# Kernel optimization log

Measured on AMD Instinct MI355X. Metric: run time of the kernel, lower is better.

The kernel has to match this reference:

```python
import jax, jax.numpy as jnp
import numpy as np

D = 384      # n_embed_dims
H = 6        # n_heads
HS = D // H  # head_size = 64
T = 256      # block_size
B = 256
EPS = 1e-5


def setup_inputs() -> dict:
    key = jax.random.key(0)
    ks = jax.random.split(key, 12)
    s_in = 1.0 / np.sqrt(D)
    s_ff = 1.0 / np.sqrt(4 * D)
    return {
        "x": jax.random.normal(ks[0], (B, T, D), jnp.float32),
        # per-head QKV weights, stacked [H, D, HS] (Linear bias=False)
        "wq": jax.random.normal(ks[1], (H, D, HS), jnp.float32) * s_in,
        "wk": jax.random.normal(ks[2], (H, D, HS), jnp.float32) * s_in,
        "wv": jax.random.normal(ks[3], (H, D, HS), jnp.float32) * s_in,
        "w_proj": jax.random.normal(ks[4], (D, D), jnp.float32) * s_in,
        "b_proj": jax.random.normal(ks[5], (D,), jnp.float32) * s_in,
        "w1": jax.random.normal(ks[6], (D, 4 * D), jnp.float32) * s_in,
        "b1": jax.random.normal(ks[7], (4 * D,), jnp.float32) * s_in,
        "w2": jax.random.normal(ks[8], (4 * D, D), jnp.float32) * s_ff,
        "b2": jax.random.normal(ks[9], (D,), jnp.float32) * s_ff,
        "g1": jnp.ones((D,), jnp.float32),
        "be1": jnp.zeros((D,), jnp.float32),
        "g2": jnp.ones((D,), jnp.float32),
        "be2": jnp.zeros((D,), jnp.float32),
    }


def _layernorm(x, g, b):
    mu = jnp.mean(x, axis=-1, keepdims=True)
    var = jnp.mean(jnp.square(x - mu), axis=-1, keepdims=True)
    return (x - mu) * jax.lax.rsqrt(var + EPS) * g + b


def _attention(x, wq, wk, wv, w_proj, b_proj):
    # faithful quirk: scale = 1/sqrt(C) with C = full embed dim (384)
    scale = 1.0 / jnp.sqrt(jnp.asarray(D, x.dtype))
    q = jnp.einsum("btd,hde->bhte", x, wq)  # [B,H,T,HS]
    k = jnp.einsum("btd,hde->bhte", x, wk)
    v = jnp.einsum("btd,hde->bhte", x, wv)
    w = jnp.einsum("bhte,bhse->bhts", q, k) * scale  # [B,H,T,T], no mask
    w = jax.nn.softmax(w, axis=-1)
    out = jnp.einsum("bhts,bhse->bhte", w, v)  # [B,H,T,HS]
    # concat heads along feature dim (head order matches torch cat)
    out = out.transpose(0, 2, 1, 3).reshape(x.shape[0], x.shape[1], D)
    return out @ w_proj + b_proj


def reference(x, wq, wk, wv, w_proj, b_proj, w1, b1, w2, b2, g1, be1, g2, be2):
    x = x + _attention(_layernorm(x, g1, be1), wq, wk, wv, w_proj, b_proj)
    h = _layernorm(x, g2, be2)
    h = jax.nn.relu(h @ w1 + b1) @ w2 + b2  # dropout = eval-mode identity
    return x + h
```

## Files before the change

### kernel.cpp

```cpp
#include <hip/hip_runtime.h>
#include <stdint.h>

#define NTOK 65536
#define DE 384
#define QSTR 1280

typedef __bf16 bf16x8 __attribute__((ext_vector_type(8)));
typedef float  f32x4  __attribute__((ext_vector_type(4)));
typedef float  f32x16 __attribute__((ext_vector_type(16)));
typedef unsigned short u16x8 __attribute__((ext_vector_type(8)));

__device__ __forceinline__ unsigned short f2bf(float f) {
  union { float fl; unsigned u; } a; a.fl = f;
  unsigned r = a.u + 0x7fffu + ((a.u >> 16) & 1u);
  return (unsigned short)(r >> 16);
}
__device__ __forceinline__ float b2f(unsigned short s) {
  union { unsigned u; float f; } v; v.u = (unsigned)s << 16; return v.f;
}

__device__ __forceinline__ void gll16(const void* g, void* l) {
  __builtin_amdgcn_global_load_lds((const __attribute__((address_space(1))) void*)g,
                                   (__attribute__((address_space(3))) void*)l, 16, 0, 0);
}

__device__ __forceinline__ bf16x8 ds128(unsigned addr) {
  bf16x8 r;
  asm volatile("ds_read_b128 %0, %1" : "=v"(r) : "v"(addr));
  return r;
}

__global__ void pack_t(unsigned short* __restrict__ dst, const float* __restrict__ src,
                       int R, int C) {
  int t = blockIdx.x * 256 + threadIdx.x;
  if (t >= R * C) return;
  int r = t / C, c = t - r * C;
  dst[(size_t)c * R + r] = f2bf(src[t]);
}

__global__ void qkv_pack(const float* __restrict__ wq, const float* __restrict__ wk,
                         const float* __restrict__ wv, unsigned short* __restrict__ dst) {
  int t = blockIdx.x * 256 + threadIdx.x;
  if (t >= QSTR * 384) return;
  int n = t / 384, k = t - n * 384;
  unsigned short v = 0;
  if (n < 1152) {
    int which = n / 384, r = n - which * 384;
    const float* src = which == 0 ? wq : (which == 1 ? wk : wv);
    int h = r >> 6, e = r & 63;
    v = f2bf(src[h * 24576 + k * 64 + e]);
  }
  dst[t] = v;
}

__global__ __launch_bounds__(256) void ln_kernel(const float* __restrict__ x,
                                                 const float* __restrict__ g,
                                                 const float* __restrict__ be,
                                                 unsigned short* __restrict__ out) {
  int wave = threadIdx.x >> 6, lane = threadIdx.x & 63;
  size_t row = (size_t)blockIdx.x * 4 + wave;
  const float* xr = x + row * DE;
  int c0 = lane * 2;
  float2 v0 = *(const float2*)(xr + c0);
  float2 v1 = *(const float2*)(xr + 128 + c0);
  float2 v2 = *(const float2*)(xr + 256 + c0);
  float s  = v0.x + v0.y + v1.x + v1.y + v2.x + v2.y;
  float ss = v0.x*v0.x + v0.y*v0.y + v1.x*v1.x + v1.y*v1.y + v2.x*v2.x + v2.y*v2.y;
#pragma unroll
  for (int m = 1; m < 64; m <<= 1) { s += __shfl_xor(s, m); ss += __shfl_xor(ss, m); }
  float mu = s * (1.0f / 384.0f);
  float rstd = rsqrtf(ss * (1.0f / 384.0f) - mu * mu + 1e-5f);
  unsigned short* orow = out + row * DE;
  {
    float a0 = (v0.x - mu) * rstd * g[c0] + be[c0];
    float a1 = (v0.y - mu) * rstd * g[c0 + 1] + be[c0 + 1];
    *(unsigned*)(orow + c0) = (unsigned)f2bf(a0) | ((unsigned)f2bf(a1) << 16);
  }
  {
    int c = c0 + 128;
    float a0 = (v1.x - mu) * rstd * g[c] + be[c];
    float a1 = (v1.y - mu) * rstd * g[c + 1] + be[c + 1];
    *(unsigned*)(orow + c) = (unsigned)f2bf(a0) | ((unsigned)f2bf(a1) << 16);
  }
  {
    int c = c0 + 256;
    float a0 = (v2.x - mu) * rstd * g[c] + be[c];
    float a1 = (v2.y - mu) * rstd * g[c + 1] + be[c + 1];
    *(unsigned*)(orow + c) = (unsigned)f2bf(a0) | ((unsigned)f2bf(a1) << 16);
  }
}

template<int EPI, int BM, int BN, int WM, int WN>
__device__ __forceinline__
void gemm_core(const unsigned short* __restrict__ A, const unsigned short* __restrict__ Bt,
               int M, int K, int Nst, int stride, int ntx,
               const float* __restrict__ bias, const float* __restrict__ residf,
               const unsigned short* __restrict__ residb,
               const float* __restrict__ g2, const float* __restrict__ be2,
               float* __restrict__ outf, unsigned short* __restrict__ outb,
               unsigned short* __restrict__ out2) {
  constexpr int T = WM * WN * 64;
  constexpr int MWT = BM / WM, NWT = BN / WN;
  constexpr int MT = MWT / 32, NT = NWT / 32;
  constexpr int LA = (BM * 128) / (T * 16);
  constexpr int LB = (BN * 128) / (T * 16);
  __shared__ __align__(16) unsigned short As[2][BM * 64];
  __shared__ __align__(16) unsigned short Bs[2][BN * 64];
  __shared__ float red[(EPI == 1) ? BM : 1][4][2];
  const int tid = threadIdx.x;
  const int wave = tid >> 6, lane = tid & 63;

  const int nwg = gridDim.x;
  const int cpx = nwg >> 3;
  const int wg = (blockIdx.x & 7) * cpx + (blockIdx.x >> 3);
  const int bx = wg % ntx, by = wg / ntx;
  const int mBase = by * BM, nBase = bx * BN;
  const int wmi = wave / WN, wni = wave % WN;
  const int wm = wmi * MWT, wn = wni * NWT;
  const int cr = lane & 31;
  const int hg = lane >> 5;

  const unsigned asb = (unsigned)(uintptr_t)&As[0][0];
  const unsigned bsb = (unsigned)(uintptr_t)&Bs[0][0];

  f32x16 acc[MT][NT];
#pragma unroll
  for (int i = 0; i < MT; ++i)
#pragma unroll
    for (int j = 0; j < NT; ++j)
#pragma unroll
      for (int r = 0; r < 16; ++r) acc[i][j][r] = 0.f;

  auto stage = [&](int buf, int kt) {
#pragma unroll
    for (int i = 0; i < LA; ++i) {
      int Lb = i * (T * 16) + wave * 1024;
      int L = Lb + lane * 16;
      int row = L >> 7;
      int col = ((((L >> 4) & 7) ^ (row & 7) ^ ((row >> 3) & 3)) << 3);
      gll16(A + (size_t)(mBase + row) * K + kt + col, (unsigned short*)As[buf] + (Lb >> 1));
    }
#pragma unroll
    for (int i = 0; i < LB; ++i) {
      int Lb = i * (T * 16) + wave * 1024;
      int L = Lb + lane * 16;
      int row = L >> 7;
      int col = ((((L >> 4) & 7) ^ (row & 7) ^ ((row >> 3) & 3)) << 3);
      gll16(Bt + (size_t)(nBase + row) * K + kt + col, (unsigned short*)Bs[buf] + (Lb >> 1));
    }
  };

  const int NK = K >> 6;
  stage(0, 0);
  for (int t = 0; t < NK; ++t) {
    const int cur = t & 1;
    if (t + 1 < NK) {
      stage(cur ^ 1, (t + 1) << 6);
      if constexpr (LA + LB == 8)      asm volatile("s_waitcnt vmcnt(8)" ::: "memory");
      else if constexpr (LA + LB == 7) asm volatile("s_waitcnt vmcnt(7)" ::: "memory");
      else                             asm volatile("s_waitcnt vmcnt(6)" ::: "memory");
    } else {
      asm volatile("s_waitcnt vmcnt(0)" ::: "memory");
    }
    asm volatile("" ::: "memory");
    __builtin_amdgcn_s_barrier();
    asm volatile("" ::: "memory");

    const unsigned ab = asb + (cur ? (unsigned)(BM * 128) : 0u);
    const unsigned bb = bsb + (cur ? (unsigned)(BN * 128) : 0u);
#pragma unroll
    for (int k2 = 0; k2 < 2; ++k2) {
      bf16x8 bfr[2][NT], af[2][MT];
#pragma unroll
      for (int kk = 0; kk < 2; ++kk) {
        const int ks = k2 * 2 + kk;
#pragma unroll
        for (int nt = 0; nt < NT; ++nt) {
          int row = wn + nt * 32 + cr;
          unsigned slot = (unsigned)(((ks * 2 + hg) ^ (row & 7) ^ ((row >> 3) & 3)) & 7);
          bfr[kk][nt] = ds128(bb + (unsigned)(row << 7) + (slot << 4));
        }
#pragma unroll
        for (int mt = 0; mt < MT; ++mt) {
          int row = wm + mt * 32 + cr;
          unsigned slot = (unsigned)(((ks * 2 + hg) ^ (row & 7) ^ ((row >> 3) & 3)) & 7);
          af[kk][mt] = ds128(ab + (unsigned)(row << 7) + (slot << 4));
        }
      }
      asm volatile("s_waitcnt lgkmcnt(0)" ::: "memory");
      __builtin_amdgcn_sched_barrier(0);
      __builtin_amdgcn_s_setprio(1);
#pragma unroll
      for (int kk = 0; kk < 2; ++kk)
#pragma unroll
        for (int mt = 0; mt < MT; ++mt)
#pragma unroll
          for (int nt = 0; nt < NT; ++nt)
            acc[mt][nt] = __builtin_amdgcn_mfma_f32_32x32x16_bf16(af[kk][mt], bfr[kk][nt],
                                                                  acc[mt][nt], 0, 0, 0);
      __builtin_amdgcn_s_setprio(0);
    }
    asm volatile("" ::: "memory");
    __builtin_amdgcn_s_barrier();
    asm volatile("" ::: "memory");
  }

  if (EPI == 1) {
#pragma unroll
    for (int mt = 0; mt < MT; ++mt) {
#pragma unroll
      for (int nt = 0; nt < NT; ++nt) {
        const int gn = nBase + wn + nt * 32 + cr;
#pragma unroll
        for (int r = 0; r < 16; ++r) {
          const int gm = mBase + wm + mt * 32 + (r & 3) + ((r >> 2) << 3) + (hg << 2);
          size_t idx = (size_t)gm * stride + gn;
          acc[mt][nt][r] = acc[mt][nt][r] + bias[gn] + residf[idx];
        }
      }
    }
#pragma unroll
    for (int mt = 0; mt < MT; ++mt) {
#pragma unroll
      for (int r = 0; r < 16; ++r) {
        float s = 0.f, ss = 0.f;
#pragma unroll
        for (int nt = 0; nt < NT; ++nt) {
          float v = acc[mt][nt][r];
          s += v; ss += v * v;
        }
        s += __shfl_xor(s, 1);  ss += __shfl_xor(ss, 1);
        s += __shfl_xor(s, 2);  ss += __shfl_xor(ss, 2);
        s += __shfl_xor(s, 4);  ss += __shfl_xor(ss, 4);
        s += __shfl_xor(s, 8);  ss += __shfl_xor(ss, 8);
        s += __shfl_xor(s, 16); ss += __shfl_xor(ss, 16);
        if (cr == 0) {
          int row = wm + mt * 32 + (r & 3) + ((r >> 2) << 3) + (hg << 2);
          red[row][wni][0] = s;
          red[row][wni][1] = ss;
        }
      }
    }
    __syncthreads();
#pragma unroll
    for (int mt = 0; mt < MT; ++mt) {
#pragma unroll
      for (int r = 0; r < 16; ++r) {
        int row = wm + mt * 32 + (r & 3) + ((r >> 2) << 3) + (hg << 2);
        float s = red[row][0][0] + red[row][1][0] + red[row][2][0] + red[row][3][0];
        float ss = red[row][0][1] + red[row][1][1] + red[row][2][1] + red[row][3][1];
        float mu = s * (1.0f / 384.0f);
        float rstd = rsqrtf(ss * (1.0f / 384.0f) - mu * mu + 1e-5f);
        const int gm = mBase + row;
#pragma unroll
        for (int nt = 0; nt < NT; ++nt) {
          const int gn = nBase + wn + nt * 32 + cr;
          size_t idx = (size_t)gm * stride + gn;
          float x1v = acc[mt][nt][r];
          outb[idx] = f2bf(x1v);
          out2[idx] = f2bf((x1v - mu) * rstd * g2[gn] + be2[gn]);
        }
      }
    }
    return;
  }

#pragma unroll
  for (int mt = 0; mt < MT; ++mt) {
#pragma unroll
    for (int nt = 0; nt < NT; ++nt) {
      const int gn = nBase + wn + nt * 32 + cr;
      if (gn < Nst) {
#pragma unroll
        for (int r = 0; r < 16; ++r) {
          const int gm = mBase + wm + mt * 32 + (r & 3) + ((r >> 2) << 3) + (hg << 2);
          float val = acc[mt][nt][r];
          size_t idx = (size_t)gm * stride + gn;
          if (EPI == 0) {
            outb[idx] = f2bf(val);
          } else if (EPI == 2) {
            float rr = val + bias[gn];
            outb[idx] = f2bf(rr > 0.f ? rr : 0.f);
          } else {
            outf[idx] = val + bias[gn] + b2f(residb[idx]);
          }
        }
      }
    }
  }
}

__global__ __launch_bounds__(512, 1)
void gemm_qkv(const unsigned short* __restrict__ A, const unsigned short* __restrict__ Bt,
              int M, int K, int Nst, int stride, int ntx,
              const float* __restrict__ bias, const float* __restrict__ residf,
              const unsigned short* __restrict__ residb, float* __restrict__ outf,
              unsigned short* __restrict__ outb) {
  gemm_core<0, 256, 192, 4, 2>(A, Bt, M, K, Nst, stride, ntx, bias, residf, residb,
                               nullptr, nullptr, outf, outb, nullptr);
}
__global__ __launch_bounds__(512, 1)
void gemm_projln(const unsigned short* __restrict__ A, const unsigned short* __restrict__ Bt,
                 int M, int K, int Nst, int stride, int ntx,
                 const float* __restrict__ bias, const float* __restrict__ residf,
                 const float* __restrict__ g2, const float* __restrict__ be2,
                 unsigned short* __restrict__ outb, unsigned short* __restrict__ out2) {
  gemm_core<1, 128, 384, 2, 4>(A, Bt, M, K, Nst, stride, ntx, bias, residf, nullptr,
                               g2, be2, nullptr, outb, out2);
}
__global__ __launch_bounds__(512, 1)
void gemm_mlp1(const unsigned short* __restrict__ A, const unsigned short* __restrict__ Bt,
               int M, int K, int Nst, int stride, int ntx,
               const float* __restrict__ bias, const float* __restrict__ residf,
               const unsigned short* __restrict__ residb, float* __restrict__ outf,
               unsigned short* __restrict__ outb) {
  gemm_core<2, 256, 256, 2, 4>(A, Bt, M, K, Nst, stride, ntx, bias, residf, residb,
                               nullptr, nullptr, outf, outb, nullptr);
}
__global__ __launch_bounds__(512, 1)
void gemm_mlp2(const unsigned short* __restrict__ A, const unsigned short* __restrict__ Bt,
               int M, int K, int Nst, int stride, int ntx,
               const float* __restrict__ bias, const float* __restrict__ residf,
               const unsigned short* __restrict__ residb, float* __restrict__ outf,
               unsigned short* __restrict__ outb) {
  gemm_core<3, 256, 128, 4, 2>(A, Bt, M, K, Nst, stride, ntx, bias, residf, residb,
                               nullptr, nullptr, outf, outb, nullptr);
}

__global__ __launch_bounds__(256)
void attn_kernel(const unsigned short* __restrict__ qkvn, unsigned short* __restrict__ o) {
  __shared__ unsigned short Vt[64 * 256];
  __shared__ unsigned short Pw[4][64 * 32];
  const int bh = blockIdx.x;
  const int b = bh / 6, h = bh - b * 6;
  const unsigned short* base = qkvn + (size_t)(b * 256) * QSTR;
  const unsigned short* qb = base + h * 64;
  const unsigned short* kbp = base + 384 + h * 64;
  const unsigned short* vbp = base + 768 + h * 64;
  const int wave = threadIdx.x >> 6, lane = threadIdx.x & 63;
  const int fr = lane & 15, fg = lane >> 4;
  const int fk = fg << 3;
  const int qrow0 = wave << 6;
  const float scale = 0.051031036307982884f;
  const f32x4 z = {0.f, 0.f, 0.f, 0.f};

  {
    const int s = threadIdx.x;
    u16x8 v8[8];
#pragma unroll
    for (int j = 0; j < 8; ++j)
      v8[j] = *(const u16x8*)(vbp + (size_t)s * QSTR + j * 8);
#pragma unroll
    for (int e = 0; e < 64; ++e)
      Vt[(e << 8) + (s ^ ((e & 7) << 3))] = v8[e >> 3][e & 7];
  }
  __syncthreads();

  bf16x8 qf[4][2];
#pragma unroll
  for (int rb = 0; rb < 4; ++rb)
#pragma unroll
    for (int ks = 0; ks < 2; ++ks)
      qf[rb][ks] = *(const bf16x8*)(qb + (size_t)(qrow0 + rb * 16 + fr) * QSTR + ks * 32 + fk);

  f32x4 oacc[4][4];
  float psum[4][4];
#pragma unroll
  for (int rb = 0; rb < 4; ++rb)
#pragma unroll
    for (int nb = 0; nb < 4; ++nb) oacc[rb][nb] = z;
#pragma unroll
  for (int rb = 0; rb < 4; ++rb)
#pragma unroll
    for (int i = 0; i < 4; ++i) psum[rb][i] = 0.f;

  for (int kb2 = 0; kb2 < 8; ++kb2) {
#pragma unroll
    for (int c2 = 0; c2 < 2; ++c2) {
      int cb = kb2 * 2 + c2;
      bf16x8 kf0 = *(const bf16x8*)(kbp + (size_t)(cb * 16 + fr) * QSTR + fk);
      bf16x8 kf1 = *(const bf16x8*)(kbp + (size_t)(cb * 16 + fr) * QSTR + 32 + fk);
#pragma unroll
      for (int rb = 0; rb < 4; ++rb) {
        f32x4 s = __builtin_amdgcn_mfma_f32_16x16x32_bf16(qf[rb][0], kf0, z, 0, 0, 0);
        s = __builtin_amdgcn_mfma_f32_16x16x32_bf16(qf[rb][1], kf1, s, 0, 0, 0);
#pragma unroll
        for (int i = 0; i < 4; ++i) {
          float p = __expf(fminf(scale * s[i], 60.f));
          psum[rb][i] += p;
          Pw[wave][(rb * 16 + (fg << 2) + i) * 32 + c2 * 16 + fr] = f2bf(p);
        }
      }
    }
    bf16x8 pa[4], vf[4];
#pragma unroll
    for (int rb = 0; rb < 4; ++rb) pa[rb] = *(const bf16x8*)(&Pw[wave][(rb * 16 + fr) * 32 + fk]);
#pragma unroll
    for (int nb = 0; nb < 4; ++nb) {
      int e = nb * 16 + fr;
      vf[nb] = *(const bf16x8*)(&Vt[(e << 8) + ((kb2 * 32 + fk) ^ ((e & 7) << 3))]);
    }
#pragma unroll
    for (int rb = 0; rb < 4; ++rb)
#pragma unroll
      for (int nb = 0; nb < 4; ++nb)
        oacc[rb][nb] = __builtin_amdgcn_mfma_f32_16x16x32_bf16(pa[rb], vf[nb], oacc[rb][nb], 0, 0, 0);
  }

  float rs[4][4];
#pragma unroll
  for (int rb = 0; rb < 4; ++rb)
#pragma unroll
    for (int i = 0; i < 4; ++i) {
      float v = psum[rb][i];
      v += __shfl_xor(v, 1);
      v += __shfl_xor(v, 2);
      v += __shfl_xor(v, 4);
      v += __shfl_xor(v, 8);
      rs[rb][i] = 1.0f / v;
    }

#pragma unroll
  for (int rb = 0; rb < 4; ++rb)
#pragma unroll
    for (int nb = 0; nb < 4; ++nb)
#pragma unroll
      for (int i = 0; i < 4; ++i) {
        int token = b * 256 + qrow0 + rb * 16 + (fg << 2) + i;
        int gcol = h * 64 + nb * 16 + fr;
        o[(size_t)token * DE + gcol] = f2bf(oacc[rb][nb][i] * rs[rb][i]);
      }
}

extern "C" void kernel_launch(void* const* d_in, const int* in_sizes, int n_in,
                              void* d_out, int out_size, void* d_ws, size_t ws_size,
                              hipStream_t stream) {
  const float* x     = (const float*)d_in[0];
  const float* wq    = (const float*)d_in[1];
  const float* wk    = (const float*)d_in[2];
  const float* wv    = (const float*)d_in[3];
  const float* wproj = (const float*)d_in[4];
  const float* bproj = (const float*)d_in[5];
  const float* w1    = (const float*)d_in[6];
  const float* b1    = (const float*)d_in[7];
  const float* w2    = (const float*)d_in[8];
  const float* b2    = (const float*)d_in[9];
  const float* g1    = (const float*)d_in[10];
  const float* be1   = (const float*)d_in[11];
  const float* g2    = (const float*)d_in[12];
  const float* be2   = (const float*)d_in[13];

  char* ws = (char*)d_ws;
  unsigned short* xln   = (unsigned short*)(ws + 0);
  unsigned short* x1b   = (unsigned short*)(ws + 0);
  unsigned short* qkvn  = (unsigned short*)(ws + 50331648);
  unsigned short* hbuf  = (unsigned short*)(ws + 100663296);
  unsigned short* act   = (unsigned short*)(ws + 150994944);
  unsigned short* attno = (unsigned short*)(ws + 218103808);
  unsigned short* wqkvt = (unsigned short*)(ws + 352321536);
  unsigned short* wprjt = (unsigned short*)(ws + 352321536 + 983040);
  unsigned short* w1t   = (unsigned short*)(ws + 352321536 + 983040 + 294912);
  unsigned short* w2t   = (unsigned short*)(ws + 352321536 + 983040 + 294912 + 1179648);

  qkv_pack<<<(QSTR * 384 + 255) / 256, 256, 0, stream>>>(wq, wk, wv, wqkvt);
  pack_t<<<(147456 + 255) / 256, 256, 0, stream>>>(wprjt, wproj, 384, 384);
  pack_t<<<(589824 + 255) / 256, 256, 0, stream>>>(w1t, w1, 384, 1536);
  pack_t<<<(589824 + 255) / 256, 256, 0, stream>>>(w2t, w2, 1536, 384);

  ln_kernel<<<NTOK / 4, 256, 0, stream>>>(x, g1, be1, xln);

  gemm_qkv<<<6 * 256, 512, 0, stream>>>(xln, wqkvt, NTOK, 384, 1152, 1280, 6,
                                        nullptr, nullptr, nullptr, nullptr, qkvn);

  attn_kernel<<<1536, 256, 0, stream>>>(qkvn, attno);

  gemm_projln<<<512, 512, 0, stream>>>(attno, wprjt, NTOK, 384, 384, 384, 1,
                                       bproj, x, g2, be2, x1b, hbuf);

  gemm_mlp1<<<6 * 256, 512, 0, stream>>>(hbuf, w1t, NTOK, 384, 1536, 1536, 6,
                                         b1, nullptr, nullptr, nullptr, act);

  gemm_mlp2<<<3 * 256, 512, 0, stream>>>(act, w2t, NTOK, 1536, 384, 384, 3,
                                         b2, nullptr, x1b, (float*)d_out, nullptr);
}
```

Before: 516.6 us.

## Use 512x192 GEMM tiles with K=32 staging for QKV and MLP GEMMs

```diff
diff --git a/kernel.cpp b/kernel.cpp
--- a/kernel.cpp
+++ b/kernel.cpp
@@ -90,23 +90,14 @@
   }
 }
 
-template<int EPI, int BM, int BN, int WM, int WN>
+template<int EPI>
 __device__ __forceinline__
-void gemm_core(const unsigned short* __restrict__ A, const unsigned short* __restrict__ Bt,
-               int M, int K, int Nst, int stride, int ntx,
-               const float* __restrict__ bias, const float* __restrict__ residf,
-               const unsigned short* __restrict__ residb,
-               const float* __restrict__ g2, const float* __restrict__ be2,
-               float* __restrict__ outf, unsigned short* __restrict__ outb,
-               unsigned short* __restrict__ out2) {
-  constexpr int T = WM * WN * 64;
-  constexpr int MWT = BM / WM, NWT = BN / WN;
-  constexpr int MT = MWT / 32, NT = NWT / 32;
-  constexpr int LA = (BM * 128) / (T * 16);
-  constexpr int LB = (BN * 128) / (T * 16);
-  __shared__ __align__(16) unsigned short As[2][BM * 64];
-  __shared__ __align__(16) unsigned short Bs[2][BN * 64];
-  __shared__ float red[(EPI == 1) ? BM : 1][4][2];
+void gemm512_core(const unsigned short* __restrict__ A, const unsigned short* __restrict__ Bt,
+                  int K, int Nst, int stride, int ntx,
+                  const float* __restrict__ bias, const unsigned short* __restrict__ residb,
+                  float* __restrict__ outf, unsigned short* __restrict__ outb) {
+  __shared__ __align__(16) unsigned short As[2][512 * 32];
+  __shared__ __align__(16) unsigned short Bs[2][192 * 32];
   const int tid = threadIdx.x;
   const int wave = tid >> 6, lane = tid & 63;
 
@@ -114,51 +105,62 @@
   const int cpx = nwg >> 3;
   const int wg = (blockIdx.x & 7) * cpx + (blockIdx.x >> 3);
   const int bx = wg % ntx, by = wg / ntx;
-  const int mBase = by * BM, nBase = bx * BN;
-  const int wmi = wave / WN, wni = wave % WN;
-  const int wm = wmi * MWT, wn = wni * NWT;
-  const int cr = lane & 31;
-  const int hg = lane >> 5;
+  const int mBase = by << 9, nBase = bx * 192;
+  const int wm = (wave >> 1) << 7;
+  const int wn = (wave & 1) * 96;
+  const int cr = lane & 31, hg = lane >> 5;
 
   const unsigned asb = (unsigned)(uintptr_t)&As[0][0];
   const unsigned bsb = (unsigned)(uintptr_t)&Bs[0][0];
 
-  f32x16 acc[MT][NT];
-#pragma unroll
-  for (int i = 0; i < MT; ++i)
-#pragma unroll
-    for (int j = 0; j < NT; ++j)
+  f32x16 acc[4][3];
+#pragma unroll
+  for (int i = 0; i < 4; ++i)
+#pragma unroll
+    for (int j = 0; j < 3; ++j)
 #pragma unroll
       for (int r = 0; r < 16; ++r) acc[i][j][r] = 0.f;
 
-  auto stage = [&](int buf, int kt) {
-#pragma unroll
-    for (int i = 0; i < LA; ++i) {
-      int Lb = i * (T * 16) + wave * 1024;
+  auto stageA = [&](int buf, int kt, int i) {
+    int Lb = i * 8192 + wave * 1024;
+    int L = Lb + lane * 16;
+    int p = L >> 7;
+    int sl = ((L >> 4) & 7) ^ (p & 7);
+    int m = (p << 1) | (sl >> 2);
+    int col = (sl & 3) << 3;
+    gll16(A + (size_t)(mBase + m) * K + kt + col, (unsigned short*)As[buf] + (Lb >> 1));
+  };
+  auto stageB = [&](int buf, int kt, int i) {
+    int Lb = i * 8192 + wave * 1024;
+    if (Lb < 12288) {
       int L = Lb + lane * 16;
-      int row = L >> 7;
-      int col = ((((L >> 4) & 7) ^ (row & 7) ^ ((row >> 3) & 3)) << 3);
-      gll16(A + (size_t)(mBase + row) * K + kt + col, (unsigned short*)As[buf] + (Lb >> 1));
-    }
-#pragma unroll
-    for (int i = 0; i < LB; ++i) {
-      int Lb = i * (T * 16) + wave * 1024;
-      int L = Lb + lane * 16;
-      int row = L >> 7;
-      int col = ((((L >> 4) & 7) ^ (row & 7) ^ ((row >> 3) & 3)) << 3);
-      gll16(Bt + (size_t)(nBase + row) * K + kt + col, (unsigned short*)Bs[buf] + (Lb >> 1));
+      int p = L >> 7;
+      int sl = ((L >> 4) & 7) ^ (p & 7);
+      int m = (p << 1) | (sl >> 2);
+      int col = (sl & 3) << 3;
+      gll16(Bt + (size_t)(nBase + m) * K + kt + col, (unsigned short*)Bs[buf] + (Lb >> 1));
     }
   };
-
-  const int NK = K >> 6;
-  stage(0, 0);
+  auto fraddr = [&](unsigned base, int row, int s) -> unsigned {
+    return base + ((unsigned)(row >> 1) << 7) +
+           ((unsigned)((s | ((row & 1) << 2)) ^ ((row >> 1) & 7)) << 4);
+  };
+
+  const int NK = K >> 5;
+#pragma unroll
+  for (int i = 0; i < 4; ++i) stageA(0, 0, i);
+#pragma unroll
+  for (int i = 0; i < 2; ++i) stageB(0, 0, i);
+
   for (int t = 0; t < NK; ++t) {
     const int cur = t & 1;
     if (t + 1 < NK) {
-      stage(cur ^ 1, (t + 1) << 6);
-      if constexpr (LA + LB == 8)      asm volatile("s_waitcnt vmcnt(8)" ::: "memory");
-      else if constexpr (LA + LB == 7) asm volatile("s_waitcnt vmcnt(7)" ::: "memory");
-      else                             asm volatile("s_waitcnt vmcnt(6)" ::: "memory");
+      const int kt = (t + 1) << 5;
+#pragma unroll
+      for (int i = 0; i < 4; ++i) stageA(cur ^ 1, kt, i);
+#pragma unroll
+      for (int i = 0; i < 2; ++i) stageB(cur ^ 1, kt, i);
+      asm volatile("s_waitcnt vmcnt(5)" ::: "memory");
     } else {
       asm volatile("s_waitcnt vmcnt(0)" ::: "memory");
     }
@@ -166,38 +168,25 @@
     __builtin_amdgcn_s_barrier();
     asm volatile("" ::: "memory");
 
-    const unsigned ab = asb + (cur ? (unsigned)(BM * 128) : 0u);
-    const unsigned bb = bsb + (cur ? (unsigned)(BN * 128) : 0u);
-#pragma unroll
-    for (int k2 = 0; k2 < 2; ++k2) {
-      bf16x8 bfr[2][NT], af[2][MT];
-#pragma unroll
-      for (int kk = 0; kk < 2; ++kk) {
-        const int ks = k2 * 2 + kk;
-#pragma unroll
-        for (int nt = 0; nt < NT; ++nt) {
-          int row = wn + nt * 32 + cr;
-          unsigned slot = (unsigned)(((ks * 2 + hg) ^ (row & 7) ^ ((row >> 3) & 3)) & 7);
-          bfr[kk][nt] = ds128(bb + (unsigned)(row << 7) + (slot << 4));
-        }
-#pragma unroll
-        for (int mt = 0; mt < MT; ++mt) {
-          int row = wm + mt * 32 + cr;
-          unsigned slot = (unsigned)(((ks * 2 + hg) ^ (row & 7) ^ ((row >> 3) & 3)) & 7);
-          af[kk][mt] = ds128(ab + (unsigned)(row << 7) + (slot << 4));
-        }
-      }
+    const unsigned ab = asb + (cur ? 32768u : 0u);
+    const unsigned bb = bsb + (cur ? 12288u : 0u);
+#pragma unroll
+    for (int ks = 0; ks < 2; ++ks) {
+      const int s = ks * 2 + hg;
+      bf16x8 bfr[3], af[4];
+#pragma unroll
+      for (int nt = 0; nt < 3; ++nt) bfr[nt] = ds128(fraddr(bb, wn + nt * 32 + cr, s));
+#pragma unroll
+      for (int mt = 0; mt < 4; ++mt) af[mt] = ds128(fraddr(ab, wm + mt * 32 + cr, s));
       asm volatile("s_waitcnt lgkmcnt(0)" ::: "memory");
       __builtin_amdgcn_sched_barrier(0);
       __builtin_amdgcn_s_setprio(1);
 #pragma unroll
-      for (int kk = 0; kk < 2; ++kk)
-#pragma unroll
-        for (int mt = 0; mt < MT; ++mt)
-#pragma unroll
-          for (int nt = 0; nt < NT; ++nt)
-            acc[mt][nt] = __builtin_amdgcn_mfma_f32_32x32x16_bf16(af[kk][mt], bfr[kk][nt],
-                                                                  acc[mt][nt], 0, 0, 0);
+      for (int mt = 0; mt < 4; ++mt)
+#pragma unroll
+        for (int nt = 0; nt < 3; ++nt)
+          acc[mt][nt] = __builtin_amdgcn_mfma_f32_32x32x16_bf16(af[mt], bfr[nt],
+                                                                acc[mt][nt], 0, 0, 0);
       __builtin_amdgcn_s_setprio(0);
     }
     asm volatile("" ::: "memory");
@@ -205,70 +194,10 @@
     asm volatile("" ::: "memory");
   }
 
-  if (EPI == 1) {
-#pragma unroll
-    for (int mt = 0; mt < MT; ++mt) {
-#pragma unroll
-      for (int nt = 0; nt < NT; ++nt) {
-        const int gn = nBase + wn + nt * 32 + cr;
-#pragma unroll
-        for (int r = 0; r < 16; ++r) {
-          const int gm = mBase + wm + mt * 32 + (r & 3) + ((r >> 2) << 3) + (hg << 2);
-          size_t idx = (size_t)gm * stride + gn;
-          acc[mt][nt][r] = acc[mt][nt][r] + bias[gn] + residf[idx];
-        }
-      }
-    }
-#pragma unroll
-    for (int mt = 0; mt < MT; ++mt) {
-#pragma unroll
-      for (int r = 0; r < 16; ++r) {
-        float s = 0.f, ss = 0.f;
-#pragma unroll
-        for (int nt = 0; nt < NT; ++nt) {
-          float v = acc[mt][nt][r];
-          s += v; ss += v * v;
-        }
-        s += __shfl_xor(s, 1);  ss += __shfl_xor(ss, 1);
-        s += __shfl_xor(s, 2);  ss += __shfl_xor(ss, 2);
-        s += __shfl_xor(s, 4);  ss += __shfl_xor(ss, 4);
-        s += __shfl_xor(s, 8);  ss += __shfl_xor(ss, 8);
-        s += __shfl_xor(s, 16); ss += __shfl_xor(ss, 16);
-        if (cr == 0) {
-          int row = wm + mt * 32 + (r & 3) + ((r >> 2) << 3) + (hg << 2);
-          red[row][wni][0] = s;
-          red[row][wni][1] = ss;
-        }
-      }
-    }
-    __syncthreads();
-#pragma unroll
-    for (int mt = 0; mt < MT; ++mt) {
-#pragma unroll
-      for (int r = 0; r < 16; ++r) {
-        int row = wm + mt * 32 + (r & 3) + ((r >> 2) << 3) + (hg << 2);
-        float s = red[row][0][0] + red[row][1][0] + red[row][2][0] + red[row][3][0];
-        float ss = red[row][0][1] + red[row][1][1] + red[row][2][1] + red[row][3][1];
-        float mu = s * (1.0f / 384.0f);
-        float rstd = rsqrtf(ss * (1.0f / 384.0f) - mu * mu + 1e-5f);
-        const int gm = mBase + row;
-#pragma unroll
-        for (int nt = 0; nt < NT; ++nt) {
-          const int gn = nBase + wn + nt * 32 + cr;
-          size_t idx = (size_t)gm * stride + gn;
-          float x1v = acc[mt][nt][r];
-          outb[idx] = f2bf(x1v);
-          out2[idx] = f2bf((x1v - mu) * rstd * g2[gn] + be2[gn]);
-        }
-      }
-    }
-    return;
-  }
-
-#pragma unroll
-  for (int mt = 0; mt < MT; ++mt) {
-#pragma unroll
-    for (int nt = 0; nt < NT; ++nt) {
+#pragma unroll
+  for (int mt = 0; mt < 4; ++mt) {
+#pragma unroll
+    for (int nt = 0; nt < 3; ++nt) {
       const int gn = nBase + wn + nt * 32 + cr;
       if (gn < Nst) {
 #pragma unroll
@@ -290,41 +219,177 @@
   }
 }
 
-__global__ __launch_bounds__(512, 1)
+__global__ __launch_bounds__(512, 2)
 void gemm_qkv(const unsigned short* __restrict__ A, const unsigned short* __restrict__ Bt,
-              int M, int K, int Nst, int stride, int ntx,
-              const float* __restrict__ bias, const float* __restrict__ residf,
+              int K, int Nst, int stride, int ntx, const float* __restrict__ bias,
               const unsigned short* __restrict__ residb, float* __restrict__ outf,
               unsigned short* __restrict__ outb) {
-  gemm_core<0, 256, 192, 4, 2>(A, Bt, M, K, Nst, stride, ntx, bias, residf, residb,
-                               nullptr, nullptr, outf, outb, nullptr);
-}
+  gemm512_core<0>(A, Bt, K, Nst, stride, ntx, bias, residb, outf, outb);
+}
+__global__ __launch_bounds__(512, 2)
+void gemm_mlp1(const unsigned short* __restrict__ A, const unsigned short* __restrict__ Bt,
+               int K, int Nst, int stride, int ntx, const float* __restrict__ bias,
+               const unsigned short* __restrict__ residb, float* __restrict__ outf,
+               unsigned short* __restrict__ outb) {
+  gemm512_core<2>(A, Bt, K, Nst, stride, ntx, bias, residb, outf, outb);
+}
+__global__ __launch_bounds__(512, 2)
+void gemm_mlp2(const unsigned short* __restrict__ A, const unsigned short* __restrict__ Bt,
+               int K, int Nst, int stride, int ntx, const float* __restrict__ bias,
+               const unsigned short* __restrict__ residb, float* __restrict__ outf,
+               unsigned short* __restrict__ outb) {
+  gemm512_core<3>(A, Bt, K, Nst, stride, ntx, bias, residb, outf, outb);
+}
+
 __global__ __launch_bounds__(512, 1)
 void gemm_projln(const unsigned short* __restrict__ A, const unsigned short* __restrict__ Bt,
-                 int M, int K, int Nst, int stride, int ntx,
-                 const float* __restrict__ bias, const float* __restrict__ residf,
-                 const float* __restrict__ g2, const float* __restrict__ be2,
-                 unsigned short* __restrict__ outb, unsigned short* __restrict__ out2) {
-  gemm_core<1, 128, 384, 2, 4>(A, Bt, M, K, Nst, stride, ntx, bias, residf, nullptr,
-                               g2, be2, nullptr, outb, out2);
-}
-__global__ __launch_bounds__(512, 1)
-void gemm_mlp1(const unsigned short* __restrict__ A, const unsigned short* __restrict__ Bt,
-               int M, int K, int Nst, int stride, int ntx,
-               const float* __restrict__ bias, const float* __restrict__ residf,
-               const unsigned short* __restrict__ residb, float* __restrict__ outf,
-               unsigned short* __restrict__ outb) {
-  gemm_core<2, 256, 256, 2, 4>(A, Bt, M, K, Nst, stride, ntx, bias, residf, residb,
-                               nullptr, nullptr, outf, outb, nullptr);
-}
-__global__ __launch_bounds__(512, 1)
-void gemm_mlp2(const unsigned short* __restrict__ A, const unsigned short* __restrict__ Bt,
-               int M, int K, int Nst, int stride, int ntx,
-               const float* __restrict__ bias, const float* __restrict__ residf,
-               const unsigned short* __restrict__ residb, float* __restrict__ outf,
-               unsigned short* __restrict__ outb) {
-  gemm_core<3, 256, 128, 4, 2>(A, Bt, M, K, Nst, stride, ntx, bias, residf, residb,
-                               nullptr, nullptr, outf, outb, nullptr);
+                 int K, int stride, const float* __restrict__ bias,
+                 const float* __restrict__ residf, const float* __restrict__ g2,
+                 const float* __restrict__ be2, unsigned short* __restrict__ outb,
+                 unsigned short* __restrict__ out2) {
+  constexpr int BM = 128, BN = 384, WN = 4;
+  constexpr int MT = 2, NT = 3;
+  __shared__ __align__(16) unsigned short As[2][BM * 64];
+  __shared__ __align__(16) unsigned short Bs[2][BN * 64];
+  __shared__ float red[BM][4][2];
+  const int tid = threadIdx.x;
+  const int wave = tid >> 6, lane = tid & 63;
+
+  const int nwg = gridDim.x;
+  const int cpx = nwg >> 3;
+  const int wg = (blockIdx.x & 7) * cpx + (blockIdx.x >> 3);
+  const int mBase = wg * BM, nBase = 0;
+  const int wni = wave % WN;
+  const int wm = (wave / WN) * 64, wn = wni * 96;
+  const int cr = lane & 31, hg = lane >> 5;
+
+  const unsigned asb = (unsigned)(uintptr_t)&As[0][0];
+  const unsigned bsb = (unsigned)(uintptr_t)&Bs[0][0];
+
+  f32x16 acc[MT][NT];
+#pragma unroll
+  for (int i = 0; i < MT; ++i)
+#pragma unroll
+    for (int j = 0; j < NT; ++j)
+#pragma unroll
+      for (int r = 0; r < 16; ++r) acc[i][j][r] = 0.f;
+
+  auto stage = [&](int buf, int kt) {
+#pragma unroll
+    for (int i = 0; i < 2; ++i) {
+      int Lb = i * 8192 + wave * 1024;
+      int L = Lb + lane * 16;
+      int row = L >> 7;
+      int col = ((((L >> 4) & 7) ^ (row & 7) ^ ((row >> 3) & 3)) << 3);
+      gll16(A + (size_t)(mBase + row) * K + kt + col, (unsigned short*)As[buf] + (Lb >> 1));
+    }
+#pragma unroll
+    for (int i = 0; i < 6; ++i) {
+      int Lb = i * 8192 + wave * 1024;
+      int L = Lb + lane * 16;
+      int row = L >> 7;
+      int col = ((((L >> 4) & 7) ^ (row & 7) ^ ((row >> 3) & 3)) << 3);
+      gll16(Bt + (size_t)(nBase + row) * K + kt + col, (unsigned short*)Bs[buf] + (Lb >> 1));
+    }
+  };
+  auto fraddr = [&](unsigned base, int row, int s) -> unsigned {
+    return base + ((unsigned)(row << 7)) +
+           ((unsigned)((s ^ (row & 7) ^ ((row >> 3) & 3)) & 7) << 4);
+  };
+
+  const int NK = K >> 6;
+  stage(0, 0);
+  for (int t = 0; t < NK; ++t) {
+    const int cur = t & 1;
+    if (t + 1 < NK) {
+      stage(cur ^ 1, (t + 1) << 6);
+      asm volatile("s_waitcnt vmcnt(8)" ::: "memory");
+    } else {
+      asm volatile("s_waitcnt vmcnt(0)" ::: "memory");
+    }
+    asm volatile("" ::: "memory");
+    __builtin_amdgcn_s_barrier();
+    asm volatile("" ::: "memory");
+
+    const unsigned ab = asb + (cur ? (unsigned)(BM * 128) : 0u);
+    const unsigned bb = bsb + (cur ? (unsigned)(BN * 128) : 0u);
+#pragma unroll
+    for (int ks = 0; ks < 4; ++ks) {
+      const int s = ks * 2 + hg;
+      bf16x8 bfr[NT], af[MT];
+#pragma unroll
+      for (int nt = 0; nt < NT; ++nt) bfr[nt] = ds128(fraddr(bb, wn + nt * 32 + cr, s));
+#pragma unroll
+      for (int mt = 0; mt < MT; ++mt) af[mt] = ds128(fraddr(ab, wm + mt * 32 + cr, s));
+      asm volatile("s_waitcnt lgkmcnt(0)" ::: "memory");
+      __builtin_amdgcn_sched_barrier(0);
+      __builtin_amdgcn_s_setprio(1);
+#pragma unroll
+      for (int mt = 0; mt < MT; ++mt)
+#pragma unroll
+        for (int nt = 0; nt < NT; ++nt)
+          acc[mt][nt] = __builtin_amdgcn_mfma_f32_32x32x16_bf16(af[mt], bfr[nt],
+                                                                acc[mt][nt], 0, 0, 0);
+      __builtin_amdgcn_s_setprio(0);
+    }
+    asm volatile("" ::: "memory");
+    __builtin_amdgcn_s_barrier();
+    asm volatile("" ::: "memory");
+  }
+
+#pragma unroll
+  for (int mt = 0; mt < MT; ++mt)
+#pragma unroll
+    for (int nt = 0; nt < NT; ++nt) {
+      const int gn = nBase + wn + nt * 32 + cr;
+#pragma unroll
+      for (int r = 0; r < 16; ++r) {
+        const int gm = mBase + wm + mt * 32 + (r & 3) + ((r >> 2) << 3) + (hg << 2);
+        size_t idx = (size_t)gm * stride + gn;
+        acc[mt][nt][r] = acc[mt][nt][r] + bias[gn] + residf[idx];
+      }
+    }
+#pragma unroll
+  for (int mt = 0; mt < MT; ++mt)
+#pragma unroll
+    for (int r = 0; r < 16; ++r) {
+      float s = 0.f, ss = 0.f;
+#pragma unroll
+      for (int nt = 0; nt < NT; ++nt) {
+        float v = acc[mt][nt][r];
+        s += v; ss += v * v;
+      }
+      s += __shfl_xor(s, 1);  ss += __shfl_xor(ss, 1);
+      s += __shfl_xor(s, 2);  ss += __shfl_xor(ss, 2);
+      s += __shfl_xor(s, 4);  ss += __shfl_xor(ss, 4);
+      s += __shfl_xor(s, 8);  ss += __shfl_xor(ss, 8);
+      s += __shfl_xor(s, 16); ss += __shfl_xor(ss, 16);
+      if (cr == 0) {
+        int row = wm + mt * 32 + (r & 3) + ((r >> 2) << 3) + (hg << 2);
+        red[row][wni][0] = s;
+        red[row][wni][1] = ss;
+      }
+    }
+  __syncthreads();
+#pragma unroll
+  for (int mt = 0; mt < MT; ++mt)
+#pragma unroll
+    for (int r = 0; r < 16; ++r) {
+      int row = wm + mt * 32 + (r & 3) + ((r >> 2) << 3) + (hg << 2);
+      float s = red[row][0][0] + red[row][1][0] + red[row][2][0] + red[row][3][0];
+      float ss = red[row][0][1] + red[row][1][1] + red[row][2][1] + red[row][3][1];
+      float mu = s * (1.0f / 384.0f);
+      float rstd = rsqrtf(ss * (1.0f / 384.0f) - mu * mu + 1e-5f);
+      const int gm = mBase + row;
+#pragma unroll
+      for (int nt = 0; nt < NT; ++nt) {
+        const int gn = nBase + wn + nt * 32 + cr;
+        size_t idx = (size_t)gm * stride + gn;
+        float x1v = acc[mt][nt][r];
+        outb[idx] = f2bf(x1v);
+        out2[idx] = f2bf((x1v - mu) * rstd * g2[gn] + be2[gn]);
+      }
+    }
 }
 
 __global__ __launch_bounds__(256)
@@ -469,17 +534,17 @@
 
   ln_kernel<<<NTOK / 4, 256, 0, stream>>>(x, g1, be1, xln);
 
-  gemm_qkv<<<6 * 256, 512, 0, stream>>>(xln, wqkvt, NTOK, 384, 1152, 1280, 6,
-                                        nullptr, nullptr, nullptr, nullptr, qkvn);
+  gemm_qkv<<<128 * 6, 512, 0, stream>>>(xln, wqkvt, 384, 1152, 1280, 6,
+                                        nullptr, nullptr, nullptr, qkvn);
 
   attn_kernel<<<1536, 256, 0, stream>>>(qkvn, attno);
 
-  gemm_projln<<<512, 512, 0, stream>>>(attno, wprjt, NTOK, 384, 384, 384, 1,
+  gemm_projln<<<512, 512, 0, stream>>>(attno, wprjt, 384, 384,
                                        bproj, x, g2, be2, x1b, hbuf);
 
-  gemm_mlp1<<<6 * 256, 512, 0, stream>>>(hbuf, w1t, NTOK, 384, 1536, 1536, 6,
-                                         b1, nullptr, nullptr, nullptr, act);
-
-  gemm_mlp2<<<3 * 256, 512, 0, stream>>>(act, w2t, NTOK, 1536, 384, 384, 3,
-                                         b2, nullptr, x1b, (float*)d_out, nullptr);
-}
+  gemm_mlp1<<<128 * 8, 512, 0, stream>>>(hbuf, w1t, 384, 1536, 1536, 8,
+                                         b1, nullptr, nullptr, act);
+
+  gemm_mlp2<<<128 * 2, 512, 0, stream>>>(act, w2t, 1536, 384, 384, 2,
+                                         b2, x1b, (float*)d_out, nullptr);
+}
```

New measurement: 519.0 us. About the same (+0.5%).
